# Kernel optimization log

Hardware: AMD Instinct MI355X
Metric: run time of the kernel (lower is better)

## Reference

```python
import jax, jax.numpy as jnp
import numpy as np


def setup_inputs() -> dict:
    key = jax.random.key(0)
    k1, k2, k3, k4 = jax.random.split(key, 4)
    B, C, H, W = 16, 64, 128, 128
    x = jax.random.normal(k1, (B, C, H, W), dtype=jnp.float32)
    y = jax.random.normal(k2, (B, C, H, W), dtype=jnp.float32)
    # nn.Parameter(torch.zeros(1)) in the original; use small random values so
    # the attention branch contributes (zeros would make it a pure residual).
    temperature1 = jax.random.normal(k3, (1,), dtype=jnp.float32) * 0.1
    temperature2 = jax.random.normal(k4, (1,), dtype=jnp.float32) * 0.1
    return {"x": x, "y": y, "temperature1": temperature1,
            "temperature2": temperature2, "num_heads": 4}


def _l2norm_lastdim(v):
    # F.normalize(v, dim=-1): v / max(||v||_2, eps)
    n = jnp.sqrt(jnp.sum(v * v, axis=-1, keepdims=True))
    return v / jnp.maximum(n, 1e-12)


def reference(x, y, temperature1, temperature2, num_heads):
    B, C, H, W = x.shape
    c = C // num_heads
    HW = H * W
    # b (head c) h w -> b head c (h w)
    xr = x.reshape(B, num_heads, c, HW)
    yr = y.reshape(B, num_heads, c, HW)

    # key_x normalized over (h w); key_y (b head (hw) c) normalized over dim=-2,
    # which is the same (h w) axis of yr in 'bhck' layout.
    key_x = _l2norm_lastdim(xr)
    key_y = _l2norm_lastdim(yr)
    # energy[b,h,c,d] = sum_k key_x[b,h,c,k] * key_y[b,h,d,k]  -> (B, head, c, c)
    energy = jnp.einsum('bhck,bhdk->bhcd', key_x, key_y)

    attn1 = jax.nn.softmax(energy, axis=-1)                        # (B,h,c,c)
    attn2 = jax.nn.softmax(energy.transpose(0, 1, 3, 2), axis=-1)  # (B,h,c,c)

    # y_att (b head (hw) c) = value_y @ attn1, then 'b head (h w) c -> b (head c) h w'
    # out[b,h,d,k] = sum_c attn1[b,h,c,d] * yr[b,h,c,k]
    y_att = jnp.einsum('bhcd,bhck->bhdk', attn1, yr).reshape(B, C, H, W)
    x_att = jnp.einsum('bhcd,bhck->bhdk', attn2, xr).reshape(B, C, H, W)

    y_ = temperature1[0] * y_att + x
    x_ = temperature2[0] * x_att + y
    return jnp.concatenate((x_, y_), axis=1)  # (B, 2C, H, W)
```

## Files before the change

kernel.cpp:

```cpp
#include <hip/hip_runtime.h>

#define HW      16384
#define CPH     16
#define NBH     64
#define NSLICE  16
#define KSLICE  (HW / NSLICE)
#define TKT     256
#define LS      260
#define KPT     4
#define PSTRIDE 288


__global__ __launch_bounds__(256) void gram_kernel(
    const float* __restrict__ x,
    const float* __restrict__ y,
    float* __restrict__ ws)
{
    __shared__ float xs[16 * LS];
    __shared__ float ys[16 * LS];
    __shared__ float Gs[256];
    __shared__ float sxs[16], sys[16];

    const int blk = blockIdx.x;
    const int bh  = blk >> 4;
    const int sl  = blk & 15;
    const int ks  = sl * KSLICE;
    const int t   = threadIdx.x;

    Gs[t] = 0.f;
    if (t < 16) { sxs[t] = 0.f; sys[t] = 0.f; }

    const int c0 = t & 3;
    const int d0 = (t >> 2) & 3;
    const int g  = t >> 4;

    float acc[4][4];
    #pragma unroll
    for (int i = 0; i < 4; ++i)
        #pragma unroll
        for (int j = 0; j < 4; ++j) acc[i][j] = 0.f;
    float sqx[4] = {0.f, 0.f, 0.f, 0.f};
    float sqy[4] = {0.f, 0.f, 0.f, 0.f};

    const float* xb = x + (size_t)bh * CPH * HW + ks;
    const float* yb = y + (size_t)bh * CPH * HW + ks;

    for (int kt = 0; kt < KSLICE; kt += TKT) {
        __syncthreads();
        #pragma unroll
        for (int i = 0; i < 4; ++i) {
            int idx = i * 256 + t;
            int row = idx >> 6;
            int col = (idx & 63) * 4;
            float4 xv = *reinterpret_cast<const float4*>(xb + (size_t)row * HW + kt + col);
            float4 yv = *reinterpret_cast<const float4*>(yb + (size_t)row * HW + kt + col);
            *reinterpret_cast<float4*>(&xs[row * LS + col]) = xv;
            *reinterpret_cast<float4*>(&ys[row * LS + col]) = yv;
        }
        __syncthreads();

        #pragma unroll
        for (int kq = 0; kq < 16; kq += 4) {
            float4 xr[4], yr[4];
            #pragma unroll
            for (int i = 0; i < 4; ++i)
                xr[i] = *reinterpret_cast<const float4*>(&xs[(c0 + 4 * i) * LS + g * 16 + kq]);
            #pragma unroll
            for (int j = 0; j < 4; ++j)
                yr[j] = *reinterpret_cast<const float4*>(&ys[(d0 + 4 * j) * LS + g * 16 + kq]);
            #pragma unroll
            for (int i = 0; i < 4; ++i)
                #pragma unroll
                for (int j = 0; j < 4; ++j) {
                    acc[i][j] = fmaf(xr[i].x, yr[j].x, acc[i][j]);
                    acc[i][j] = fmaf(xr[i].y, yr[j].y, acc[i][j]);
                    acc[i][j] = fmaf(xr[i].z, yr[j].z, acc[i][j]);
                    acc[i][j] = fmaf(xr[i].w, yr[j].w, acc[i][j]);
                }
            if (d0 == 0) {
                #pragma unroll
                for (int i = 0; i < 4; ++i) {
                    sqx[i] = fmaf(xr[i].x, xr[i].x, sqx[i]);
                    sqx[i] = fmaf(xr[i].y, xr[i].y, sqx[i]);
                    sqx[i] = fmaf(xr[i].z, xr[i].z, sqx[i]);
                    sqx[i] = fmaf(xr[i].w, xr[i].w, sqx[i]);
                }
            }
            if (c0 == 0) {
                #pragma unroll
                for (int j = 0; j < 4; ++j) {
                    sqy[j] = fmaf(yr[j].x, yr[j].x, sqy[j]);
                    sqy[j] = fmaf(yr[j].y, yr[j].y, sqy[j]);
                    sqy[j] = fmaf(yr[j].z, yr[j].z, sqy[j]);
                    sqy[j] = fmaf(yr[j].w, yr[j].w, sqy[j]);
                }
            }
        }
    }

    #pragma unroll
    for (int i = 0; i < 4; ++i)
        #pragma unroll
        for (int j = 0; j < 4; ++j)
            atomicAdd(&Gs[(c0 + 4 * i) * 16 + (d0 + 4 * j)], acc[i][j]);
    if (d0 == 0) {
        #pragma unroll
        for (int i = 0; i < 4; ++i) atomicAdd(&sxs[c0 + 4 * i], sqx[i]);
    }
    if (c0 == 0) {
        #pragma unroll
        for (int j = 0; j < 4; ++j) atomicAdd(&sys[d0 + 4 * j], sqy[j]);
    }
    __syncthreads();

    float* P = ws + (size_t)(bh * NSLICE + sl) * PSTRIDE;
    P[t] = Gs[t];
    if (t < 16)       P[256 + t] = sxs[t];
    else if (t < 32)  P[272 + (t - 16)] = sys[t - 16];
}

__global__ __launch_bounds__(256) void apply_kernel(
    const float* __restrict__ x,
    const float* __restrict__ y,
    const float* __restrict__ ws,
    const float* __restrict__ t1p,
    const float* __restrict__ t2p,
    float* __restrict__ out)
{
    const int CHUNKS = HW / (256 * KPT);
    const int blk   = blockIdx.x;
    const int bh    = blk / CHUNKS;
    const int chunk = blk % CHUNKS;
    const int t     = threadIdx.x;
    const int k0    = chunk * (256 * KPT) + t * KPT;
    const int i     = t >> 4;
    const int j     = t & 15;

    __shared__ float  Es[256];
    __shared__ float2 Ws[256];
    __shared__ float  nxs[16], nys[16];

    const float* P = ws + (size_t)bh * NSLICE * PSTRIDE;
    float gsum = 0.f;
    #pragma unroll
    for (int s = 0; s < NSLICE; ++s) gsum += P[s * PSTRIDE + t];
    if (t < 32) {
        const int off = (t < 16) ? (256 + t) : (272 + (t - 16));
        float q = 0.f;
        #pragma unroll
        for (int s = 0; s < NSLICE; ++s) q += P[s * PSTRIDE + off];
        float n = fmaxf(sqrtf(q), 1e-12f);
        if (t < 16) nxs[t] = n; else nys[t - 16] = n;
    }
    __syncthreads();

    const float e = gsum / (nxs[i] * nys[j]);
    Es[t] = e;
    __syncthreads();

    float rm = -1e30f;
    #pragma unroll
    for (int r = 0; r < 16; ++r) rm = fmaxf(rm, Es[i * 16 + r]);
    float rs = 0.f;
    #pragma unroll
    for (int r = 0; r < 16; ++r) rs += expf(Es[i * 16 + r] - rm);
    const float a1 = expf(e - rm) / rs;

    float cm = -1e30f;
    #pragma unroll
    for (int r = 0; r < 16; ++r) cm = fmaxf(cm, Es[r * 16 + j]);
    float cs = 0.f;
    #pragma unroll
    for (int r = 0; r < 16; ++r) cs += expf(Es[r * 16 + j] - cm);
    const float v2 = expf(e - cm) / cs;

    const float t1 = t1p[0];
    const float t2 = t2p[0];
    float* Wsf = reinterpret_cast<float*>(Ws);
    Wsf[(i * 16 + j) * 2 + 1] = t1 * a1;
    Wsf[(j * 16 + i) * 2 + 0] = t2 * v2;
    __syncthreads();

    const int b = bh >> 2;
    const int h = bh & 3;

    const float* xbase = x + ((size_t)bh * CPH) * HW + k0;
    const float* ybase = y + ((size_t)bh * CPH) * HW + k0;

    float accx[16][KPT];
    float accy[16][KPT];
    #pragma unroll
    for (int d = 0; d < 16; ++d)
        #pragma unroll
        for (int q = 0; q < KPT; ++q) { accx[d][q] = 0.f; accy[d][q] = 0.f; }

    float4 xq = *reinterpret_cast<const float4*>(xbase);
    float4 yq = *reinterpret_cast<const float4*>(ybase);
    #pragma unroll
    for (int c = 0; c < 16; ++c) {
        float4 xn, yn;
        if (c < 15) {
            xn = *reinterpret_cast<const float4*>(xbase + (size_t)(c + 1) * HW);
            yn = *reinterpret_cast<const float4*>(ybase + (size_t)(c + 1) * HW);
        }
        float xv[KPT] = {xq.x, xq.y, xq.z, xq.w};
        float yv[KPT] = {yq.x, yq.y, yq.z, yq.w};
        #pragma unroll
        for (int d = 0; d < 16; ++d) {
            float2 w = Ws[c * 16 + d];
            #pragma unroll
            for (int q = 0; q < KPT; ++q) accx[d][q] = fmaf(w.x, xv[q], accx[d][q]);
            #pragma unroll
            for (int q = 0; q < KPT; ++q) accy[d][q] = fmaf(w.y, yv[q], accy[d][q]);
        }
        #pragma unroll
        for (int q = 0; q < KPT; ++q) accx[c][q] += yv[q];
        #pragma unroll
        for (int q = 0; q < KPT; ++q) accy[c][q] += xv[q];
        xq = xn; yq = yn;
    }

    const size_t obx = ((size_t)b * 128 + h * 16) * HW + k0;
    const size_t oby = obx + (size_t)64 * HW;
    #pragma unroll
    for (int d = 0; d < 16; ++d) {
        float4 px = make_float4(accx[d][0], accx[d][1], accx[d][2], accx[d][3]);
        float4 py = make_float4(accy[d][0], accy[d][1], accy[d][2], accy[d][3]);
        *reinterpret_cast<float4*>(out + obx + (size_t)d * HW) = px;
        *reinterpret_cast<float4*>(out + oby + (size_t)d * HW) = py;
    }
}

extern "C" void kernel_launch(void* const* d_in, const int* in_sizes, int n_in,
                              void* d_out, int out_size, void* d_ws, size_t ws_size,
                              hipStream_t stream) {
    const float* x  = (const float*)d_in[0];
    const float* y  = (const float*)d_in[1];
    const float* t1 = (const float*)d_in[2];
    const float* t2 = (const float*)d_in[3];
    float* ws  = (float*)d_ws;
    float* out = (float*)d_out;

    gram_kernel<<<NBH * NSLICE, 256, 0, stream>>>(x, y, ws);
    apply_kernel<<<NBH * (HW / (256 * KPT)), 256, 0, stream>>>(x, y, ws, t1, t2, out);
}
```

Measured before the change: 291.2 us.

## Use direct global-to-LDS loads in gram kernel and halve apply per-thread work

The gram kernel now stages x/y tiles with global_load_lds, which writes global data straight into shared memory and skips the register round trip. The apply kernel processes 2 elements per thread instead of 4, which doubles the grid and reduces register pressure, and it drops the manual software prefetch. Both kernels add launch_bounds occupancy hints of 4. The risks are narrower float2 memory accesses, weaker load pipelining in apply, and whether the LDS-direct load places data at the expected per-lane offsets.

```diff
diff --git a/kernel.cpp b/kernel.cpp
--- a/kernel.cpp
+++ b/kernel.cpp
@@ -7,11 +7,11 @@
 #define KSLICE  (HW / NSLICE)
 #define TKT     256
 #define LS      260
-#define KPT     4
+#define KPT     2
 #define PSTRIDE 288
 
 
-__global__ __launch_bounds__(256) void gram_kernel(
+__global__ __launch_bounds__(256, 4) void gram_kernel(
     const float* __restrict__ x,
     const float* __restrict__ y,
     float* __restrict__ ws)
@@ -21,11 +21,13 @@
     __shared__ float Gs[256];
     __shared__ float sxs[16], sys[16];
 
-    const int blk = blockIdx.x;
-    const int bh  = blk >> 4;
-    const int sl  = blk & 15;
-    const int ks  = sl * KSLICE;
-    const int t   = threadIdx.x;
+    const int blk  = blockIdx.x;
+    const int bh   = blk >> 4;
+    const int sl   = blk & 15;
+    const int ks   = sl * KSLICE;
+    const int t    = threadIdx.x;
+    const int lane = t & 63;
+    const int wv   = t >> 6;
 
     Gs[t] = 0.f;
     if (t < 16) { sxs[t] = 0.f; sys[t] = 0.f; }
@@ -49,13 +51,17 @@
         __syncthreads();
         #pragma unroll
         for (int i = 0; i < 4; ++i) {
-            int idx = i * 256 + t;
-            int row = idx >> 6;
-            int col = (idx & 63) * 4;
-            float4 xv = *reinterpret_cast<const float4*>(xb + (size_t)row * HW + kt + col);
-            float4 yv = *reinterpret_cast<const float4*>(yb + (size_t)row * HW + kt + col);
-            *reinterpret_cast<float4*>(&xs[row * LS + col]) = xv;
-            *reinterpret_cast<float4*>(&ys[row * LS + col]) = yv;
+            const int row = i * 4 + wv;
+            const float* gx = xb + (size_t)row * HW + kt + lane * 4;
+            const float* gy = yb + (size_t)row * HW + kt + lane * 4;
+            __builtin_amdgcn_global_load_lds(
+                (const __attribute__((address_space(1))) unsigned int*)gx,
+                (__attribute__((address_space(3))) unsigned int*)&xs[row * LS],
+                16, 0, 0);
+            __builtin_amdgcn_global_load_lds(
+                (const __attribute__((address_space(1))) unsigned int*)gy,
+                (__attribute__((address_space(3))) unsigned int*)&ys[row * LS],
+                16, 0, 0);
         }
         __syncthreads();
 
@@ -119,7 +125,7 @@
     else if (t < 32)  P[272 + (t - 16)] = sys[t - 16];
 }
 
-__global__ __launch_bounds__(256) void apply_kernel(
+__global__ __launch_bounds__(256, 4) void apply_kernel(
     const float* __restrict__ x,
     const float* __restrict__ y,
     const float* __restrict__ ws,
@@ -194,40 +200,28 @@
         #pragma unroll
         for (int q = 0; q < KPT; ++q) { accx[d][q] = 0.f; accy[d][q] = 0.f; }
 
-    float4 xq = *reinterpret_cast<const float4*>(xbase);
-    float4 yq = *reinterpret_cast<const float4*>(ybase);
     #pragma unroll
     for (int c = 0; c < 16; ++c) {
-        float4 xn, yn;
-        if (c < 15) {
-            xn = *reinterpret_cast<const float4*>(xbase + (size_t)(c + 1) * HW);
-            yn = *reinterpret_cast<const float4*>(ybase + (size_t)(c + 1) * HW);
-        }
-        float xv[KPT] = {xq.x, xq.y, xq.z, xq.w};
-        float yv[KPT] = {yq.x, yq.y, yq.z, yq.w};
+        float2 xv = *reinterpret_cast<const float2*>(xbase + (size_t)c * HW);
+        float2 yv = *reinterpret_cast<const float2*>(ybase + (size_t)c * HW);
         #pragma unroll
         for (int d = 0; d < 16; ++d) {
             float2 w = Ws[c * 16 + d];
-            #pragma unroll
-            for (int q = 0; q < KPT; ++q) accx[d][q] = fmaf(w.x, xv[q], accx[d][q]);
-            #pragma unroll
-            for (int q = 0; q < KPT; ++q) accy[d][q] = fmaf(w.y, yv[q], accy[d][q]);
+            accx[d][0] = fmaf(w.x, xv.x, accx[d][0]);
+            accx[d][1] = fmaf(w.x, xv.y, accx[d][1]);
+            accy[d][0] = fmaf(w.y, yv.x, accy[d][0]);
+            accy[d][1] = fmaf(w.y, yv.y, accy[d][1]);
         }
-        #pragma unroll
-        for (int q = 0; q < KPT; ++q) accx[c][q] += yv[q];
-        #pragma unroll
-        for (int q = 0; q < KPT; ++q) accy[c][q] += xv[q];
-        xq = xn; yq = yn;
+        accx[c][0] += yv.x;  accx[c][1] += yv.y;
+        accy[c][0] += xv.x;  accy[c][1] += xv.y;
     }
 
     const size_t obx = ((size_t)b * 128 + h * 16) * HW + k0;
     const size_t oby = obx + (size_t)64 * HW;
     #pragma unroll
     for (int d = 0; d < 16; ++d) {
-        float4 px = make_float4(accx[d][0], accx[d][1], accx[d][2], accx[d][3]);
-        float4 py = make_float4(accy[d][0], accy[d][1], accy[d][2], accy[d][3]);
-        *reinterpret_cast<float4*>(out + obx + (size_t)d * HW) = px;
-        *reinterpret_cast<float4*>(out + oby + (size_t)d * HW) = py;
+        *reinterpret_cast<float2*>(out + obx + (size_t)d * HW) = make_float2(accx[d][0], accx[d][1]);
+        *reinterpret_cast<float2*>(out + oby + (size_t)d * HW) = make_float2(accy[d][0], accy[d][1]);
     }
 }
 
```

Measured after the change: 477.8 us. +64.1%, slower.
